# Kernel optimization log

Measured on AMD Instinct MI355X. Metric: run time of the kernel, lower is better.

The kernel has to match this reference:

```python
import jax, jax.numpy as jnp
import numpy as np

B, T, F, D, H, DFF, L = 8, 1024, 64, 512, 8, 2048, 3
DH = D // H
PERIODS = np.array([16, 256, 4096], np.int32)
CMS_LRS = np.array([0.01, 0.001, 0.0001], np.float32)
TITANS_LR = 0.01
TITANS_CLIP = 0.1


def layernorm(x, w, b):
    m = x.mean(-1, keepdims=True)
    v = x.var(-1, keepdims=True)
    return (x - m) * jax.lax.rsqrt(v + 1e-5) * w + b


def setup_inputs() -> dict:
    key = jax.random.key(0)
    ks = jax.random.split(key, 40)
    f32 = jnp.float32
    def rn(i, shape, s=0.02):
        return jax.random.normal(ks[i], shape, f32) * s
    inp = {
        'x': jax.random.normal(ks[0], (B, T, F), f32),
        'titans_W': jnp.zeros((D, D), f32),
        'cms_summary': jnp.zeros((L, D), f32),
        'cms_buf_sum': jnp.zeros((L, D), f32),
        'cms_count': jnp.zeros((L,), jnp.int32),
        'cms_step': jnp.zeros((L,), jnp.int32),
        'in_norm_w': jnp.ones((F,), f32), 'in_norm_b': jnp.zeros((F,), f32),
        'in_proj_W': rn(1, (D, F)), 'in_proj_b': jnp.zeros((D,), f32),
        'W_base': rn(2, (D, D), 0.01),
        'tit_out_W': rn(3, (D, D)), 'tit_out_b': jnp.zeros((D,), f32),
        'gate_W': rn(4, (L, D, D)), 'gate_b': jnp.zeros((L, D), f32),
        'comb_W': rn(5, (D, L * D)), 'comb_b': jnp.zeros((D,), f32),
        'n1_w': jnp.ones((D,), f32), 'n1_b': jnp.zeros((D,), f32),
        'qkv_W': rn(6, (3 * D, D)), 'qkv_b': jnp.zeros((3 * D,), f32),
        'ao_W': rn(7, (D, D)), 'ao_b': jnp.zeros((D,), f32),
        'n2_w': jnp.ones((D,), f32), 'n2_b': jnp.zeros((D,), f32),
        'f1_W': rn(8, (DFF, D)), 'f1_b': jnp.zeros((DFF,), f32),
        'f2_W': rn(9, (D, DFF)), 'f2_b': jnp.zeros((D,), f32),
        'fn_w': jnp.ones((D,), f32), 'fn_b': jnp.zeros((D,), f32),
        'head_W': rn(10, (1, D)), 'head_b': jnp.zeros((1,), f32),
    }
    return inp


def cms_tick_all(means, summary, buf_sum, count, step, gate_W, gate_b):
    """Sequential tick over T timesteps, vectorized over the L levels.
    means: [T, D] batch-mean of final hidden at each timestep."""
    periods = jnp.asarray(PERIODS)
    lrs = jnp.asarray(CMS_LRS)
    def step_fn(carry, m):
        summ, bs, cnt, stp = carry
        bs = bs + m[None, :]              # [L, D]
        cnt = cnt + 1
        stp = stp + 1
        fire = cnt >= periods              # [L]
        acc = bs / cnt.astype(bs.dtype)[:, None]
        g = jax.nn.sigmoid(jnp.einsum('lij,lj->li', gate_W, acc) + gate_b)
        new_summ = jnp.where(fire[:, None], (1.0 - lrs)[:, None] * summ + lrs[:, None] * g * acc, summ)
        bs = jnp.where(fire[:, None], jnp.zeros_like(bs), bs)
        cnt = jnp.where(fire, jnp.zeros_like(cnt), cnt)
        return (new_summ, bs, cnt, stp), None
    (summary, buf_sum, count, step), _ = jax.lax.scan(step_fn, (summary, buf_sum, count, step), means)
    return summary, buf_sum, count, step


def reference(x, titans_W, cms_summary, cms_buf_sum, cms_count, cms_step,
              in_norm_w, in_norm_b, in_proj_W, in_proj_b,
              W_base, tit_out_W, tit_out_b,
              gate_W, gate_b, comb_W, comb_b,
              n1_w, n1_b, qkv_W, qkv_b, ao_W, ao_b,
              n2_w, n2_b, f1_W, f1_b, f2_W, f2_b,
              fn_w, fn_b, head_W, head_b):
    # input norm + projection: [B,T,F] -> [B,T,D]
    h = layernorm(x, in_norm_w, in_norm_b) @ in_proj_W.T + in_proj_b
    # Titans fast-weight read
    W = W_base + titans_W
    tit = (h @ W.T) @ tit_out_W.T + tit_out_b
    # Titans fast-weight update (detached in the original)
    hs = jax.lax.stop_gradient(h)
    target = hs.mean(axis=1)               # [B, D]
    query = hs[:, -1, :]                   # [B, D]
    pred_m = query @ titans_W.T
    err = (target - pred_m).mean(axis=0)   # [D]
    grad = jnp.outer(err, query.mean(axis=0))
    gn = jnp.linalg.norm(grad)
    grad = jnp.where(gn > TITANS_CLIP, grad * (TITANS_CLIP / gn), grad)
    new_W = titans_W + TITANS_LR * grad
    h = h + tit
    # CMS residual from current summaries: concat [L*D] -> combine -> [D]
    cms_out = cms_summary.reshape(L * D) @ comb_W.T + comb_b
    h = h + cms_out                        # broadcast over [B,T,D]
    # transformer block (pre-norm, causal MHA)
    hn = layernorm(h, n1_w, n1_b)
    qkv = hn @ qkv_W.T + qkv_b
    q, k, v = jnp.split(qkv, 3, axis=-1)
    def to_heads(t):
        return t.reshape(B, T, H, DH).transpose(0, 2, 1, 3)
    q, k, v = to_heads(q), to_heads(k), to_heads(v)
    scores = jnp.einsum('bhqd,bhkd->bhqk', q, k) / np.sqrt(DH).astype(np.float32)
    causal = jnp.triu(jnp.ones((T, T), bool), 1)
    scores = jnp.where(causal, -jnp.inf, scores)
    attn = jax.nn.softmax(scores, axis=-1)
    ao = jnp.einsum('bhqk,bhkd->bhqd', attn, v).transpose(0, 2, 1, 3).reshape(B, T, D)
    h = h + ao @ ao_W.T + ao_b
    hn2 = layernorm(h, n2_w, n2_b)
    h = h + jax.nn.gelu(hn2 @ f1_W.T + f1_b, approximate=False) @ f2_W.T + f2_b
    h = layernorm(h, fn_w, fn_b)
    pred = (h @ head_W.T + head_b).squeeze(-1)   # [B, T]
    # CMS tick over all T steps (detached in the original)
    means = jax.lax.stop_gradient(h).mean(axis=0)  # [T, D]
    ns, nb, nc, nt = cms_tick_all(means, cms_summary, cms_buf_sum, cms_count, cms_step, gate_W, gate_b)
    return pred, new_W, ns, nb, nc, nt
```

## Files before the change

kernel.cpp:

```cpp
#include <hip/hip_runtime.h>
#include <hip/hip_bf16.h>
#include <math.h>

#define Bdim 8
#define Tdim 1024
#define Fdim 64
#define Ddim 512
#define Lcms 3

#define OFF_PRED 0
#define OFF_W    8192
#define OFF_NS   270336
#define OFF_NB   271872
#define OFF_NC   273408
#define OFF_NT   273411

typedef __hip_bfloat16 bf16;
typedef __attribute__((ext_vector_type(8))) short s8;
typedef __attribute__((ext_vector_type(4))) float f4;

__device__ __forceinline__ float b2f(bf16 v){ return __bfloat162float(v); }
__device__ __forceinline__ bf16  f2b(float v){ return __float2bfloat16(v); }
__device__ __forceinline__ short fb16(float v){ bf16 t = __float2bfloat16(v); return *reinterpret_cast<short*>(&t); }
__device__ __forceinline__ float toF(float v){ return v; }
__device__ __forceinline__ float toF(bf16 v){ return __bfloat162float(v); }
template<typename T> __device__ __forceinline__ T fromF(float v);
template<> __device__ __forceinline__ float fromF<float>(float v){ return v; }
template<> __device__ __forceinline__ bf16  fromF<bf16 >(float v){ return f2b(v); }

__device__ __forceinline__ f4 mfma16(s8 a, s8 b, f4 c){
  return __builtin_amdgcn_mfma_f32_16x16x32_bf16(a, b, c, 0, 0, 0);
}

__device__ __forceinline__ void gload16(const bf16* g, bf16* l){
  __builtin_amdgcn_global_load_lds(
      (const __attribute__((address_space(1))) unsigned*)g,
      (__attribute__((address_space(3))) unsigned*)l, 16, 0, 0);
}

__device__ __forceinline__ float gelu_fast(float x){
  float z2 = 1.5957691216f*(x + 0.044715f*x*x*x);
  z2 = fminf(fmaxf(z2, -18.f), 18.f);
  return x / (1.f + __expf(-z2));
}

__global__ __launch_bounds__(256) void k_conv_all(
    const void* s0, const void* s1, const void* s2, const void* s3,
    const void* s4, const void* s5, const void* s6, const void* s7,
    const void* s8v, const void* s9, const void* s10, const void* s11,
    const void* s12, const void* s13,
    bf16* __restrict__ dst, const unsigned* __restrict__ w1, int* __restrict__ flag,
    const int* __restrict__ cnt, int* __restrict__ params){
  bool isbf = (w1[0] == 0x3F803F80u);
  if (blockIdx.x==0 && threadIdx.x==0){
    flag[0] = isbf ? 1 : 0;
    const int P[3] = {16,256,4096};
    for (int l=0;l<3;l++){
      int c0 = cnt[l];
      int t1 = P[l] - c0 - 1; if (t1 < 0) t1 = 0;
      int K = (t1 >= Tdim) ? 0 : 1 + (Tdim-1-t1)/P[l];
      params[l*4+0]=t1; params[l*4+1]=K; params[l*4+2]=c0+t1+1; params[l*4+3]=c0;
    }
  }
  const void* srcs[14] = {s0,s1,s2,s3,s4,s5,s6,s7,s8v,s9,s10,s11,s12,s13};
  const int   ns[14]   = {262144,512,786432,1536,262144,512,1048576,2048,1048576,512,
                          32768,512,786432,1536};
  int gstride = gridDim.x*blockDim.x;
  int gid = blockIdx.x*blockDim.x + threadIdx.x;
  int base = 0;
  #pragma unroll
  for (int s=0;s<14;s++){
    int n = ns[s];
    if (isbf){
      const short* sp = (const short*)srcs[s]; short* dp = (short*)(dst+base);
      for (int i=gid;i<n;i+=gstride) dp[i] = sp[i];
    } else {
      const float* sp = (const float*)srcs[s];
      for (int i=gid;i<n;i+=gstride) dst[base+i] = f2b(sp[i]);
    }
    base += n;
  }
}

template<typename TW>
__device__ __forceinline__ void lnx_impl(const TW* x, const TW* nw, const TW* nb_, bf16* xn){
  int row = blockIdx.x*4 + (threadIdx.x>>6);
  int lane = threadIdx.x & 63;
  float v = toF(x[(size_t)row*Fdim + lane]);
  float s = v, s2 = v*v;
  #pragma unroll
  for (int off=32; off; off>>=1){ s += __shfl_down(s,off); s2 += __shfl_down(s2,off); }
  s = __shfl(s, 0); s2 = __shfl(s2, 0);
  float mu = s*(1.f/64.f);
  float var = s2*(1.f/64.f) - mu*mu;
  float rstd = rsqrtf(var + 1e-5f);
  xn[(size_t)row*Fdim + lane] = f2b((v-mu)*rstd*toF(nw[lane]) + toF(nb_[lane]));
}
__global__ __launch_bounds__(256) void k_lnx(const void* x, const void* nw, const void* nb_,
    bf16* xn, const int* flg){
  if (*flg) lnx_impl<bf16>((const bf16*)x,(const bf16*)nw,(const bf16*)nb_,xn);
  else      lnx_impl<float>((const float*)x,(const float*)nw,(const float*)nb_,xn);
}

__global__ __launch_bounds__(256) void k_reduce_tq1(const bf16* __restrict__ h,
    float* __restrict__ redtmp){
  int b = blockIdx.x>>5, chunk = blockIdx.x&31;
  int tid = threadIdx.x;
  #pragma unroll
  for (int o=0;o<2;o++){
    int d = tid + o*256;
    const bf16* p = h + ((size_t)b*Tdim + chunk*32)*Ddim + d;
    float s = 0.f;
    #pragma unroll
    for (int t=0;t<32;t++) s += b2f(p[(size_t)t*Ddim]);
    redtmp[((size_t)b*32 + chunk)*Ddim + d] = s;
  }
}

template<typename TW>
__device__ __forceinline__ void misc1_impl(const TW* Wbse, const TW* tW, bf16* Wout,
    const TW* summ, const TW* combW, const TW* combb, float* outv,
    const bf16* h, const float* redtmp, float* target, float* query){
  int blk = blockIdx.x, tid = threadIdx.x;
  if (blk < 1024){
    int i = blk*256 + tid;
    Wout[i] = f2b(toF(Wbse[i]) + toF(tW[i]));
  } else if (blk < 1152){
    __shared__ float s_s[Lcms*Ddim];
    for (int i=tid;i<Lcms*Ddim;i+=256) s_s[i] = toF(summ[i]);
    __syncthreads();
    int wave = tid>>6, lane = tid&63;
    int d = (blk-1024)*4 + wave;
    const TW* wr = combW + (size_t)d*(Lcms*Ddim);
    float a = 0.f;
    for (int j=lane;j<Lcms*Ddim;j+=64) a += s_s[j]*toF(wr[j]);
    #pragma unroll
    for (int off=32; off; off>>=1) a += __shfl_down(a,off);
    if (lane==0) outv[d] = a + toF(combb[d]);
  } else {
    int i = (blk-1152)*256 + tid;
    int b = i>>9, d = i&511;
    float s = 0.f;
    #pragma unroll
    for (int c=0;c<32;c++) s += redtmp[((size_t)b*32+c)*Ddim + d];
    target[i] = s*(1.f/(float)Tdim);
    query[i]  = b2f(h[((size_t)b*Tdim + (Tdim-1))*Ddim + d]);
  }
}
__global__ __launch_bounds__(256) void k_misc1(const void* Wbse, const void* tW, bf16* Wout,
    const void* summ, const void* combW, const void* combb, float* outv,
    const bf16* h, const float* redtmp, float* target, float* query, const int* flg){
  if (*flg) misc1_impl<bf16>((const bf16*)Wbse,(const bf16*)tW,Wout,(const bf16*)summ,
                             (const bf16*)combW,(const bf16*)combb,outv,h,redtmp,target,query);
  else      misc1_impl<float>((const float*)Wbse,(const float*)tW,Wout,(const float*)summ,
                             (const float*)combW,(const float*)combb,outv,h,redtmp,target,query);
}

template<typename TW>
__device__ __forceinline__ void titans_err_impl(const float* target, const float* query,
    const TW* tW, float* err, float* qmean){
  int wave = threadIdx.x>>6, lane = threadIdx.x&63;
  int d = blockIdx.x*4 + wave;
  const TW* wr = tW + (size_t)d*Ddim;
  float s = 0.f;
  #pragma unroll
  for (int b=0;b<Bdim;b++){
    const float* q = query + b*Ddim;
    float p = 0.f;
    for (int j=lane;j<Ddim;j+=64) p += q[j]*toF(wr[j]);
    s += p;
  }
  #pragma unroll
  for (int off=32; off; off>>=1) s += __shfl_down(s,off);
  if (lane==0){
    float e=0.f, qm=0.f;
    #pragma unroll
    for (int b=0;b<Bdim;b++){ e += target[b*Ddim+d]; qm += query[b*Ddim+d]; }
    err[d]   = (e - s)*(1.f/(float)Bdim);
    qmean[d] = qm*(1.f/(float)Bdim);
  }
}
__global__ __launch_bounds__(256) void k_titans_err(const float* target, const float* query,
    const void* tW, float* err, float* qmean, const int* flg){
  if (*flg) titans_err_impl<bf16>(target,query,(const bf16*)tW,err,qmean);
  else      titans_err_impl<float>(target,query,(const float*)tW,err,qmean);
}

template<typename TW>
__device__ __forceinline__ void new_W_impl(const TW* tW, const float* err, const float* qmean,
    TW* outW){
  int tid = threadIdx.x;
  float a = err[tid]*err[tid] + err[tid+256]*err[tid+256];
  float b = qmean[tid]*qmean[tid] + qmean[tid+256]*qmean[tid+256];
  #pragma unroll
  for (int off=32; off; off>>=1){ a += __shfl_down(a,off); b += __shfl_down(b,off); }
  __shared__ float sa[4], sb[4];
  int lane = tid & 63, wid = tid >> 6;
  if (lane==0){ sa[wid]=a; sb[wid]=b; }
  __syncthreads();
  float A = sa[0]+sa[1]+sa[2]+sa[3];
  float Bq= sb[0]+sb[1]+sb[2]+sb[3];
  float gn = sqrtf(A*Bq);
  float sf = 0.01f * (gn > 0.1f ? 0.1f/gn : 1.0f);
  int i = blockIdx.x*256 + tid;
  int r = i >> 9, c = i & 511;
  outW[i] = fromF<TW>(toF(tW[i]) + sf*err[r]*qmean[c]);
}
__global__ __launch_bounds__(256) void k_new_W(const void* tW, const float* err,
    const float* qmean, void* out, const int* flg){
  if (*flg) new_W_impl<bf16>((const bf16*)tW, err, qmean, ((bf16*)out)+OFF_W);
  else      new_W_impl<float>((const float*)tW, err, qmean, ((float*)out)+OFF_W);
}

template<int MODE, int DEPTH>
__global__ __launch_bounds__(512) void gemm_mfma(const bf16* __restrict__ A,
    const bf16* __restrict__ Bw, const bf16* __restrict__ bias,
    const float* __restrict__ colvec, bf16* __restrict__ Cout,
    const bf16* __restrict__ resid, int M, int N, int K){
  __shared__ __align__(16) bf16 As[DEPTH][128*32];
  __shared__ __align__(16) bf16 Bs[DEPTH][128*32];
  int tid = threadIdx.x, wave = tid>>6, lane = tid&63, quad = lane>>4, l16 = lane&15;
  int row0 = blockIdx.x*128, col0 = blockIdx.y*128;
  int wr = (wave>>2)*64, wc = (wave&3)*32;
  int srow = wave*16 + (lane>>2);
  int scol = (((lane&3) ^ ((lane>>3)&3)))*8;
  int rswz = (quad ^ ((l16>>1)&3))*8;
  f4 acc[8] = {};
  int niter = K >> 5;
  #define STAGE(bu, k0) { \
    gload16(A  + (size_t)(row0 + srow)*K + (k0) + scol, &As[bu][wave*512 + lane*8]); \
    gload16(Bw + (size_t)(col0 + srow)*K + (k0) + scol, &Bs[bu][wave*512 + lane*8]); \
  }
  STAGE(0, 0)
  if (DEPTH >= 3 && niter > 1) STAGE(1, 32)
  if (DEPTH >= 4 && niter > 2) STAGE(2, 64)
  for (int k=0; k<niter; k++){
    int bu = k & (DEPTH-1);
    if (DEPTH == 2){
      if (k+1 < niter){
        STAGE((k+1)&1, (k+1)<<5)
        asm volatile("s_waitcnt vmcnt(2)" ::: "memory");
      } else {
        asm volatile("s_waitcnt vmcnt(0)" ::: "memory");
      }
    } else {
      if (k+3 < niter){
        STAGE((k+3)&3, (k+3)<<5)
        asm volatile("s_waitcnt vmcnt(6)" ::: "memory");
      } else if (k+2 < niter){
        asm volatile("s_waitcnt vmcnt(4)" ::: "memory");
      } else if (k+1 < niter){
        asm volatile("s_waitcnt vmcnt(2)" ::: "memory");
      } else {
        asm volatile("s_waitcnt vmcnt(0)" ::: "memory");
      }
    }
    __builtin_amdgcn_s_barrier();
    s8 af[4], bfv[2];
    #pragma unroll
    for (int i=0;i<4;i++) af[i]  = *reinterpret_cast<const s8*>(&As[bu][(wr + i*16 + l16)*32 + rswz]);
    #pragma unroll
    for (int j=0;j<2;j++) bfv[j] = *reinterpret_cast<const s8*>(&Bs[bu][(wc + j*16 + l16)*32 + rswz]);
    #pragma unroll
    for (int i=0;i<4;i++)
      #pragma unroll
      for (int j=0;j<2;j++)
        acc[i*2+j] = mfma16(af[i], bfv[j], acc[i*2+j]);
    asm volatile("s_waitcnt lgkmcnt(0)" ::: "memory");
    __builtin_amdgcn_s_barrier();
  }
  #undef STAGE
  #pragma unroll
  for (int i=0;i<4;i++){
    #pragma unroll
    for (int j=0;j<2;j++){
      int n = col0 + wc + j*16 + l16;
      f4 a = acc[i*2+j];
      #pragma unroll
      for (int r=0;r<4;r++){
        int m = row0 + wr + i*16 + quad*4 + r;
        float v = a[r];
        if (MODE & 1) v += b2f(bias[n]);
        if (MODE & 8) v += colvec[n];
        if (MODE & 4) v = gelu_fast(v);
        if (MODE & 2) v += b2f(resid[(size_t)m*Ddim + n]);
        Cout[(size_t)m*N + n] = f2b(v);
      }
    }
  }
}

template<typename TW, int HEAD>
__device__ __forceinline__ void ln_impl(const bf16* in, const TW* w, const TW* b, bf16* outp,
    const TW* hw, const TW* hb, TW* pred){
  int row = blockIdx.x;
  const bf16* r = in + (size_t)row*Ddim;
  int tid = threadIdx.x;
  float v0 = b2f(r[tid]), v1 = b2f(r[tid + 256]);
  float s = v0+v1, s2 = v0*v0 + v1*v1;
  #pragma unroll
  for (int off=32; off; off>>=1){ s += __shfl_down(s,off); s2 += __shfl_down(s2,off); }
  __shared__ float sa[4], sb[4], sc[4];
  int lane = tid & 63, wid = tid >> 6;
  if (lane==0){ sa[wid]=s; sb[wid]=s2; }
  __syncthreads();
  float ts  = sa[0]+sa[1]+sa[2]+sa[3];
  float ts2 = sb[0]+sb[1]+sb[2]+sb[3];
  float mu = ts*(1.f/(float)Ddim);
  float var = ts2*(1.f/(float)Ddim) - mu*mu;
  float rstd = rsqrtf(var + 1e-5f);
  float o0 = (v0-mu)*rstd*toF(w[tid])     + toF(b[tid]);
  float o1 = (v1-mu)*rstd*toF(w[tid+256]) + toF(b[tid+256]);
  outp[(size_t)row*Ddim + tid]       = f2b(o0);
  outp[(size_t)row*Ddim + tid + 256] = f2b(o1);
  if (HEAD){
    float sp = o0*toF(hw[tid]) + o1*toF(hw[tid+256]);
    #pragma unroll
    for (int off=32; off; off>>=1) sp += __shfl_down(sp,off);
    if (lane==0) sc[wid] = sp;
    __syncthreads();
    if (tid==0) pred[row] = fromF<TW>(sc[0]+sc[1]+sc[2]+sc[3] + toF(hb[0]));
  }
}
template<int HEAD>
__global__ __launch_bounds__(256) void k_ln(const bf16* in, const void* w, const void* b,
    bf16* outp, const void* hw, const void* hb, void* out, const int* flg){
  if (*flg) ln_impl<bf16,HEAD>(in,(const bf16*)w,(const bf16*)b,outp,
                               (const bf16*)hw,(const bf16*)hb,((bf16*)out)+OFF_PRED);
  else      ln_impl<float,HEAD>(in,(const float*)w,(const float*)b,outp,
                               (const float*)hw,(const float*)hb,((float*)out)+OFF_PRED);
}

__global__ __launch_bounds__(256) void k_attn_mfma(const bf16* __restrict__ qkv,
                                                   bf16* __restrict__ ao){
  int blk = blockIdx.x;
  int bh = blk & 63;
  int qt = 15 - (blk >> 6);
  int head = bh & 7, b = bh >> 3;
  __shared__ __align__(16) bf16 Ks[64][72];
  __shared__ __align__(16) unsigned Vt4[64*36];
  __shared__ __align__(16) bf16 Ps[4][16][72];
  int tid = threadIdx.x, wave = tid>>6, lane = tid&63, quad = lane>>4, l16 = lane&15;
  int q0w = qt*64 + wave*16;
  const bf16* basep = qkv + (size_t)b*Tdim*1536 + head*64;
  s8 qf0 = *reinterpret_cast<const s8*>(basep + (size_t)(q0w+l16)*1536 + quad*8);
  s8 qf1 = *reinterpret_cast<const s8*>(basep + (size_t)(q0w+l16)*1536 + 32 + quad*8);
  f4 o[4] = {{0,0,0,0},{0,0,0,0},{0,0,0,0},{0,0,0,0}};
  float m_r[4] = {-3.0e38f,-3.0e38f,-3.0e38f,-3.0e38f};
  float l_r[4] = {0.f,0.f,0.f,0.f};
  int key_s = tid>>3, dgk = (tid&7)*8;
  int vp = tid>>3, dgv = (tid&7)*8;
  int vu4 = (((vp>>2) ^ (tid&7)) & 7)*4 + (vp&3);
  int nch = qt + 1;
  s8 kr0, kr1, vra, vrb;
  {
    const bf16* kp = basep + (size_t)key_s*1536 + 512 + dgk;
    kr0 = *reinterpret_cast<const s8*>(kp);
    kr1 = *reinterpret_cast<const s8*>(kp + (size_t)32*1536);
    const bf16* vpa = basep + (size_t)(2*vp)*1536 + 1024 + dgv;
    vra = *reinterpret_cast<const s8*>(vpa);
    vrb = *reinterpret_cast<const s8*>(vpa + 1536);
  }
  for (int ch=0; ch<nch; ch++){
    *reinterpret_cast<s8*>(&Ks[key_s][dgk])    = kr0;
    *reinterpret_cast<s8*>(&Ks[32+key_s][dgk]) = kr1;
    #pragma unroll
    for (int j=0;j<8;j++){
      unsigned w = (unsigned)(unsigned short)vra[j] | ((unsigned)(unsigned short)vrb[j] << 16);
      Vt4[(dgv+j)*36 + vu4] = w;
    }
    __syncthreads();
    if (ch+1 < nch){
      const bf16* kp = basep + (size_t)((ch+1)*64+key_s)*1536 + 512 + dgk;
      kr0 = *reinterpret_cast<const s8*>(kp);
      kr1 = *reinterpret_cast<const s8*>(kp + (size_t)32*1536);
      const bf16* vpa = basep + (size_t)((ch+1)*64 + 2*vp)*1536 + 1024 + dgv;
      vra = *reinterpret_cast<const s8*>(vpa);
      vrb = *reinterpret_cast<const s8*>(vpa + 1536);
    }
    f4 sc4[4] = {{0,0,0,0},{0,0,0,0},{0,0,0,0},{0,0,0,0}};
    #pragma unroll
    for (int t=0;t<4;t++){
      sc4[t] = mfma16(qf0, *reinterpret_cast<const s8*>(&Ks[t*16+l16][quad*8]),    sc4[t]);
      sc4[t] = mfma16(qf1, *reinterpret_cast<const s8*>(&Ks[t*16+l16][32+quad*8]), sc4[t]);
    }
    int key0 = ch*64 + l16;
    #pragma unroll
    for (int r=0;r<4;r++){
      int qrow = q0w + quad*4 + r;
      float a0 = (key0      <= qrow) ? sc4[0][r]*0.125f : -3.0e38f;
      float a1 = (key0 + 16 <= qrow) ? sc4[1][r]*0.125f : -3.0e38f;
      float a2 = (key0 + 32 <= qrow) ? sc4[2][r]*0.125f : -3.0e38f;
      float a3 = (key0 + 48 <= qrow) ? sc4[3][r]*0.125f : -3.0e38f;
      float mx = fmaxf(fmaxf(a0,a1), fmaxf(a2,a3));
      mx = fmaxf(mx, __shfl_xor(mx,1)); mx = fmaxf(mx, __shfl_xor(mx,2));
      mx = fmaxf(mx, __shfl_xor(mx,4)); mx = fmaxf(mx, __shfl_xor(mx,8));
      float mnew = fmaxf(m_r[r], mx);
      float al = __expf(m_r[r]-mnew); m_r[r] = mnew;
      float p0 = __expf(a0-mnew), p1 = __expf(a1-mnew);
      float p2 = __expf(a2-mnew), p3 = __expf(a3-mnew);
      float rs = (p0+p1)+(p2+p3);
      rs += __shfl_xor(rs,1); rs += __shfl_xor(rs,2);
      rs += __shfl_xor(rs,4); rs += __shfl_xor(rs,8);
      l_r[r] = l_r[r]*al + rs;
      o[0][r]*=al; o[1][r]*=al; o[2][r]*=al; o[3][r]*=al;
      int prow = quad*4+r;
      *reinterpret_cast<short*>(&Ps[wave][prow][l16])    = fb16(p0);
      *reinterpret_cast<short*>(&Ps[wave][prow][16+l16]) = fb16(p1);
      *reinterpret_cast<short*>(&Ps[wave][prow][32+l16]) = fb16(p2);
      *reinterpret_cast<short*>(&Ps[wave][prow][48+l16]) = fb16(p3);
    }
    asm volatile("s_waitcnt lgkmcnt(0)" ::: "memory");
    s8 pf0 = *reinterpret_cast<const s8*>(&Ps[wave][l16][quad*8]);
    s8 pf1 = *reinterpret_cast<const s8*>(&Ps[wave][l16][32+quad*8]);
    #pragma unroll
    for (int j=0;j<4;j++){
      int d = j*16 + l16;
      int swz = (d>>3) & 7;
      s8 b0 = *reinterpret_cast<const s8*>(&Vt4[d*36 + ((quad   ^ swz))*4]);
      s8 b1 = *reinterpret_cast<const s8*>(&Vt4[d*36 + (((4+quad)^ swz))*4]);
      o[j] = mfma16(pf0, b0, o[j]);
      o[j] = mfma16(pf1, b1, o[j]);
    }
    __syncthreads();
  }
  #pragma unroll
  for (int r=0;r<4;r++){
    float inv = 1.f/l_r[r];
    size_t rowb = (size_t)(b*Tdim + q0w + quad*4 + r)*Ddim + head*64;
    ao[rowb + l16]      = f2b(o[0][r]*inv);
    ao[rowb + 16 + l16] = f2b(o[1][r]*inv);
    ao[rowb + 32 + l16] = f2b(o[2][r]*inv);
    ao[rowb + 48 + l16] = f2b(o[3][r]*inv);
  }
}

__global__ void k_means(const bf16* __restrict__ h, float* __restrict__ means){
  int i = blockIdx.x*256 + threadIdx.x;
  float s = 0.f;
  #pragma unroll
  for (int b=0;b<Bdim;b++) s += b2f(h[(size_t)b*Tdim*Ddim + i]);
  means[i] = s*(1.f/(float)Bdim);
}

template<typename TW>
__device__ __forceinline__ void cms_acc_impl(const float* means, const TW* bs0,
    const int* params, float* acc, bf16* acch, float* tailtmp){
  int tid = threadIdx.x;
  if (blockIdx.x < 384){
    int l = blockIdx.x>>7, k = blockIdx.x&127;
    int K = params[l*4+1];
    if (k >= K){
      for (int d=tid; d<Ddim; d+=256) acch[((size_t)l*128+k)*Ddim + d] = f2b(0.f);
      return;
    }
    int t1 = params[l*4], cnt0 = params[l*4+2];
    const int P[3] = {16,256,4096};
    int lo = (k==0) ? 0 : t1 + (k-1)*P[l] + 1;
    int hi = t1 + k*P[l];
    float inv = 1.f/((k==0) ? (float)cnt0 : (float)P[l]);
    int lane = tid&63, strip = tid>>6;
    __shared__ float red[4][Ddim];
    float4 a0 = {0,0,0,0}, a1 = {0,0,0,0};
    for (int t=lo+strip; t<=hi; t+=4){
      const float4* row = (const float4*)(means + (size_t)t*Ddim);
      float4 v0 = row[lane], v1 = row[lane+64];
      a0.x+=v0.x; a0.y+=v0.y; a0.z+=v0.z; a0.w+=v0.w;
      a1.x+=v1.x; a1.y+=v1.y; a1.z+=v1.z; a1.w+=v1.w;
    }
    ((float4*)red[strip])[lane]    = a0;
    ((float4*)red[strip])[lane+64] = a1;
    __syncthreads();
    for (int d=tid; d<Ddim; d+=256){
      float s = red[0][d]+red[1][d]+red[2][d]+red[3][d];
      if (k==0) s += toF(bs0[l*Ddim+d]);
      float v = s*inv;
      acc[((size_t)l*65+k)*Ddim + d] = v;
      acch[((size_t)l*128+k)*Ddim + d] = f2b(v);
    }
  } else {
    int bb = blockIdx.x - 384;
    int l = bb>>5, chunk = bb&31;
    int t1 = params[l*4], K = params[l*4+1];
    const int P[3] = {16,256,4096};
    int lo = (K==0) ? 0 : t1 + (K-1)*P[l] + 1;
    int f = tid & 127, strip = tid >> 7;
    int tbeg = chunk*32, tend = tbeg + 32;
    if (tbeg < lo) tbeg = lo;
    float4 a = {0,0,0,0};
    for (int t=tbeg+strip; t<tend; t+=2){
      float4 v = ((const float4*)(means + (size_t)t*Ddim))[f];
      a.x+=v.x; a.y+=v.y; a.z+=v.z; a.w+=v.w;
    }
    __shared__ float4 redt[2][128];
    redt[strip][f] = a;
    __syncthreads();
    if (strip==0){
      float4 b = redt[1][f];
      a.x+=b.x; a.y+=b.y; a.z+=b.z; a.w+=b.w;
      ((float4*)(tailtmp + ((size_t)l*32 + chunk)*Ddim))[f] = a;
    }
  }
}
__global__ __launch_bounds__(256) void k_cms_acc(const float* means, const void* bs0,
    const int* params, float* acc, bf16* acch, float* tailtmp, const int* flg){
  if (*flg) cms_acc_impl<bf16>(means,(const bf16*)bs0,params,acc,acch,tailtmp);
  else      cms_acc_impl<float>(means,(const float*)bs0,params,acc,acch,tailtmp);
}

__global__ __launch_bounds__(256) void k_cms_gate_mfma(const bf16* __restrict__ accbh,
    const bf16* __restrict__ wg, const bf16* __restrict__ wgb, float* __restrict__ g){
  int l = blockIdx.y;
  const bf16* A  = accbh + (size_t)l*128*Ddim;
  const bf16* Bw = wg    + (size_t)l*Ddim*Ddim;
  __shared__ __align__(16) bf16 As[128*32];
  __shared__ __align__(16) bf16 Bs[128*32];
  int tid = threadIdx.x, wave = tid>>6, lane = tid&63, quad = lane>>4, l16 = lane&15;
  int col0 = blockIdx.x*128;
  int wr = (wave>>1)*64, wc = (wave&1)*64;
  int srow = lane>>2, scol = (lane&3)*8;
  f4 acc[16] = {};
  for (int k0=0; k0<Ddim; k0+=32){
    __syncthreads();
    #pragma unroll
    for (int it=0; it<2; it++){
      int c = wave*2 + it;
      gload16(A  + (size_t)(c*16 + srow)*Ddim + k0 + scol, &As[c*512 + lane*8]);
      gload16(Bw + (size_t)(col0 + c*16 + srow)*Ddim + k0 + scol, &Bs[c*512 + lane*8]);
    }
    __syncthreads();
    s8 af[4], bfv[4];
    #pragma unroll
    for (int i=0;i<4;i++) af[i]  = *reinterpret_cast<const s8*>(&As[(wr + i*16 + l16)*32 + quad*8]);
    #pragma unroll
    for (int j=0;j<4;j++) bfv[j] = *reinterpret_cast<const s8*>(&Bs[(wc + j*16 + l16)*32 + quad*8]);
    #pragma unroll
    for (int i=0;i<4;i++)
      #pragma unroll
      for (int j=0;j<4;j++)
        acc[i*4+j] = mfma16(af[i], bfv[j], acc[i*4+j]);
  }
  #pragma unroll
  for (int i=0;i<4;i++){
    #pragma unroll
    for (int j=0;j<4;j++){
      int n = col0 + wc + j*16 + l16;
      f4 a = acc[i*4+j];
      #pragma unroll
      for (int r=0;r<4;r++){
        int m = wr + i*16 + quad*4 + r;
        if (m < 65){
          float v = a[r] + b2f(wgb[l*Ddim + n]);
          g[((size_t)l*65 + m)*Ddim + n] = 1.f/(1.f + __expf(-v));
        }
      }
    }
  }
}

template<typename TW>
__device__ __forceinline__ void cms_final_impl(const float* acc, const float* g,
    const float* tailtmp, const TW* summ0, const TW* bs0, const int* params,
    const int* step0, TW* out){
  int l = blockIdx.x;
  int t1 = params[l*4], K = params[l*4+1], c0 = params[l*4+3];
  const int P[3] = {16,256,4096};
  const float LR[3] = {0.01f,0.001f,0.0001f};
  float lr = LR[l];
  for (int d=threadIdx.x; d<Ddim; d+=256){
    float s = toF(summ0[l*Ddim + d]);
    for (int k=0;k<K;k++)
      s = (1.f-lr)*s + lr*g[((size_t)l*65+k)*Ddim+d]*acc[((size_t)l*65+k)*Ddim+d];
    out[OFF_NS + l*Ddim + d] = fromF<TW>(s);
    float nbv = (K==0) ? toF(bs0[l*Ddim+d]) : 0.f;
    #pragma unroll
    for (int c=0;c<32;c++) nbv += tailtmp[((size_t)l*32+c)*Ddim + d];
    out[OFF_NB + l*Ddim + d] = fromF<TW>(nbv);
  }
  if (threadIdx.x==0){
    int nc = (K==0) ? c0 + Tdim : (Tdim-1 - (t1 + (K-1)*P[l]));
    out[OFF_NC + l] = fromF<TW>((float)nc);
    out[OFF_NT + l] = fromF<TW>((float)(step0[l] + Tdim));
  }
}
__global__ __launch_bounds__(256) void k_cms_final(const float* acc, const float* g,
    const float* tailtmp, const void* summ0, const void* bs0, const int* params,
    const int* step0, void* out, const int* flg){
  if (*flg) cms_final_impl<bf16>(acc,g,tailtmp,(const bf16*)summ0,(const bf16*)bs0,params,step0,(bf16*)out);
  else      cms_final_impl<float>(acc,g,tailtmp,(const float*)summ0,(const float*)bs0,params,step0,(float*)out);
}

extern "C" void kernel_launch(void* const* d_in, const int* in_sizes, int n_in,
                              void* d_out, int out_size, void* d_ws, size_t ws_size,
                              hipStream_t stream) {
  (void)in_sizes; (void)n_in; (void)out_size; (void)ws_size;
  const void* x           = d_in[0];
  const void* titansW     = d_in[1];
  const void* cms_summary = d_in[2];
  const void* cms_bufsum  = d_in[3];
  const int*  cms_count   = (const int*)d_in[4];
  const int*  cms_step    = (const int*)d_in[5];
  const void* in_norm_w   = d_in[6];
  const void* in_norm_b   = d_in[7];
  const void* in_proj_W   = d_in[8];
  const void* in_proj_b   = d_in[9];
  const void* W_base      = d_in[10];
  const void* tit_out_W   = d_in[11];
  const void* tit_out_b   = d_in[12];
  const void* gate_W      = d_in[13];
  const void* gate_b      = d_in[14];
  const void* comb_W      = d_in[15];
  const void* comb_b      = d_in[16];
  const void* n1_w        = d_in[17];
  const void* n1_b        = d_in[18];
  const void* qkv_W       = d_in[19];
  const void* qkv_b       = d_in[20];
  const void* ao_W        = d_in[21];
  const void* ao_b        = d_in[22];
  const void* n2_w        = d_in[23];
  const void* n2_b        = d_in[24];
  const void* f1_W        = d_in[25];
  const void* f1_b        = d_in[26];
  const void* f2_W        = d_in[27];
  const void* f2_b        = d_in[28];
  const void* fn_w        = d_in[29];
  const void* fn_b        = d_in[30];
  const void* head_W      = d_in[31];
  const void* head_b      = d_in[32];

  char* u8 = (char*)d_ws;
  bf16*  h     = (bf16*)(u8 + 0);
  bf16*  hnA   = (bf16*)(u8 + 8388608);
  bf16*  big   = (bf16*)(u8 + 16777216);
  bf16*  xn    = big;
  bf16*  tmid  = big + (size_t)8192*1536;
  float* means = (float*)(u8 + 50331648);
  bf16*  Wb    = (bf16*)(u8 + 52428800);
  bf16*  wall  = (bf16*)(u8 + 52953088);
  bf16*  wtit  = wall;
  bf16*  wtitb = wall + 262144;
  bf16*  wqkv  = wall + 262656;
  bf16*  wqkvb = wall + 1049088;
  bf16*  wao   = wall + 1050624;
  bf16*  waob  = wall + 1312768;
  bf16*  wf1   = wall + 1313280;
  bf16*  wf1b  = wall + 2361856;
  bf16*  wf2   = wall + 2363904;
  bf16*  wf2b  = wall + 3412480;
  bf16*  wproj = wall + 3412992;
  bf16*  wprojb= wall + 3445760;
  bf16*  wgate = wall + 3446272;
  bf16*  wgateb= wall + 4232704;
  float* target= (float*)(u8 + 61421568);
  float* query = (float*)(u8 + 61437952);
  float* errv  = (float*)(u8 + 61454336);
  float* qmean = (float*)(u8 + 61456384);
  float* cmsout= (float*)(u8 + 61458944);
  float* accb  = (float*)(u8 + 61460992);
  float* gbuf  = (float*)(u8 + 61860352);
  bf16*  accbh = (bf16*) (u8 + 62259712);
  int*   params= (int*)  (u8 + 62652928);
  int*   dflag = (int*)  (u8 + 62652992);
  float* redtmp= (float*)(u8 + 62659584);
  float* tailtmp=(float*)(u8 + 63183872);

  k_conv_all<<<1024, 256, 0, stream>>>(tit_out_W, tit_out_b, qkv_W, qkv_b, ao_W, ao_b,
                                       f1_W, f1_b, f2_W, f2_b, in_proj_W, in_proj_b,
                                       gate_W, gate_b, wall, (const unsigned*)in_norm_w,
                                       dflag, cms_count, params);
  k_lnx<<<2048, 256, 0, stream>>>(x, in_norm_w, in_norm_b, xn, dflag);
  gemm_mfma<1,2><<<dim3(64,4), 512, 0, stream>>>(xn, wproj, wprojb, nullptr, h, nullptr, 8192, 512, 64);
  k_reduce_tq1<<<256, 256, 0, stream>>>(h, redtmp);
  k_misc1<<<1168, 256, 0, stream>>>(W_base, titansW, Wb, cms_summary, comb_W, comb_b,
                                    cmsout, h, redtmp, target, query, dflag);
  k_titans_err<<<128, 256, 0, stream>>>(target, query, titansW, errv, qmean, dflag);
  k_new_W<<<1024, 256, 0, stream>>>(titansW, errv, qmean, d_out, dflag);
  gemm_mfma<0,4><<<dim3(64,4), 512, 0, stream>>>(h, Wb, nullptr, nullptr, tmid, nullptr, 8192, 512, 512);
  gemm_mfma<11,4><<<dim3(64,4), 512, 0, stream>>>(tmid, wtit, wtitb, cmsout, h, h, 8192, 512, 512);
  k_ln<0><<<8192, 256, 0, stream>>>(h, n1_w, n1_b, hnA, nullptr, nullptr, nullptr, dflag);
  gemm_mfma<1,2><<<dim3(64,12), 512, 0, stream>>>(hnA, wqkv, wqkvb, nullptr, big, nullptr, 8192, 1536, 512);
  k_attn_mfma<<<1024, 256, 0, stream>>>(big, tmid);
  gemm_mfma<3,4><<<dim3(64,4), 512, 0, stream>>>(tmid, wao, waob, nullptr, h, h, 8192, 512, 512);
  k_ln<0><<<8192, 256, 0, stream>>>(h, n2_w, n2_b, hnA, nullptr, nullptr, nullptr, dflag);
  gemm_mfma<5,2><<<dim3(64,16), 512, 0, stream>>>(hnA, wf1, wf1b, nullptr, big, nullptr, 8192, 2048, 512);
  gemm_mfma<3,4><<<dim3(64,4), 512, 0, stream>>>(big, wf2, wf2b, nullptr, h, h, 8192, 512, 2048);
  k_ln<1><<<8192, 256, 0, stream>>>(h, fn_w, fn_b, hnA, head_W, head_b, d_out, dflag);
  k_means<<<2048, 256, 0, stream>>>(hnA, means);
  k_cms_acc<<<480, 256, 0, stream>>>(means, cms_bufsum, params, accb, accbh, tailtmp, dflag);
  k_cms_gate_mfma<<<dim3(4,3), 256, 0, stream>>>(accbh, wgate, wgateb, gbuf);
  k_cms_final<<<Lcms, 256, 0, stream>>>(accb, gbuf, tailtmp, cms_summary, cms_bufsum, params, cms_step, d_out, dflag);
}
```

Before: 450.8 us.

## Process two K/V chunks per barrier in attention kernel with double LDS buffers

Restructures the flash-attention loop so two 64-key chunks are staged into LDS together and computed between a single pair of barriers, with register prefetch of the next two chunks. This halves the number of __syncthreads per key range and gives more global-load latency hiding. In exchange it doubles the K/V LDS footprint and the prefetch registers, which may reduce occupancy.

```diff
diff --git a/kernel.cpp b/kernel.cpp
--- a/kernel.cpp
+++ b/kernel.cpp
@@ -337,8 +337,8 @@
   int bh = blk & 63;
   int qt = 15 - (blk >> 6);
   int head = bh & 7, b = bh >> 3;
-  __shared__ __align__(16) bf16 Ks[64][72];
-  __shared__ __align__(16) unsigned Vt4[64*36];
+  __shared__ __align__(16) bf16 Ks[2][64][72];
+  __shared__ __align__(16) unsigned Vt4[2][64*36];
   __shared__ __align__(16) bf16 Ps[4][16][72];
   int tid = threadIdx.x, wave = tid>>6, lane = tid&63, quad = lane>>4, l16 = lane&15;
   int q0w = qt*64 + wave*16;
@@ -352,37 +352,29 @@
   int vp = tid>>3, dgv = (tid&7)*8;
   int vu4 = (((vp>>2) ^ (tid&7)) & 7)*4 + (vp&3);
   int nch = qt + 1;
-  s8 kr0, kr1, vra, vrb;
+  s8 kr0[2], kr1[2], vra[2], vrb[2];
   {
     const bf16* kp = basep + (size_t)key_s*1536 + 512 + dgk;
-    kr0 = *reinterpret_cast<const s8*>(kp);
-    kr1 = *reinterpret_cast<const s8*>(kp + (size_t)32*1536);
+    kr0[0] = *reinterpret_cast<const s8*>(kp);
+    kr1[0] = *reinterpret_cast<const s8*>(kp + (size_t)32*1536);
     const bf16* vpa = basep + (size_t)(2*vp)*1536 + 1024 + dgv;
-    vra = *reinterpret_cast<const s8*>(vpa);
-    vrb = *reinterpret_cast<const s8*>(vpa + 1536);
-  }
-  for (int ch=0; ch<nch; ch++){
-    *reinterpret_cast<s8*>(&Ks[key_s][dgk])    = kr0;
-    *reinterpret_cast<s8*>(&Ks[32+key_s][dgk]) = kr1;
-    #pragma unroll
-    for (int j=0;j<8;j++){
-      unsigned w = (unsigned)(unsigned short)vra[j] | ((unsigned)(unsigned short)vrb[j] << 16);
-      Vt4[(dgv+j)*36 + vu4] = w;
-    }
-    __syncthreads();
-    if (ch+1 < nch){
-      const bf16* kp = basep + (size_t)((ch+1)*64+key_s)*1536 + 512 + dgk;
-      kr0 = *reinterpret_cast<const s8*>(kp);
-      kr1 = *reinterpret_cast<const s8*>(kp + (size_t)32*1536);
-      const bf16* vpa = basep + (size_t)((ch+1)*64 + 2*vp)*1536 + 1024 + dgv;
-      vra = *reinterpret_cast<const s8*>(vpa);
-      vrb = *reinterpret_cast<const s8*>(vpa + 1536);
-    }
+    vra[0] = *reinterpret_cast<const s8*>(vpa);
+    vrb[0] = *reinterpret_cast<const s8*>(vpa + 1536);
+    if (1 < nch){
+      const bf16* kp1 = basep + (size_t)(64+key_s)*1536 + 512 + dgk;
+      kr0[1] = *reinterpret_cast<const s8*>(kp1);
+      kr1[1] = *reinterpret_cast<const s8*>(kp1 + (size_t)32*1536);
+      const bf16* vpa1 = basep + (size_t)(64 + 2*vp)*1536 + 1024 + dgv;
+      vra[1] = *reinterpret_cast<const s8*>(vpa1);
+      vrb[1] = *reinterpret_cast<const s8*>(vpa1 + 1536);
+    }
+  }
+  auto do_chunk = [&](int ch, int bu){
     f4 sc4[4] = {{0,0,0,0},{0,0,0,0},{0,0,0,0},{0,0,0,0}};
     #pragma unroll
     for (int t=0;t<4;t++){
-      sc4[t] = mfma16(qf0, *reinterpret_cast<const s8*>(&Ks[t*16+l16][quad*8]),    sc4[t]);
-      sc4[t] = mfma16(qf1, *reinterpret_cast<const s8*>(&Ks[t*16+l16][32+quad*8]), sc4[t]);
+      sc4[t] = mfma16(qf0, *reinterpret_cast<const s8*>(&Ks[bu][t*16+l16][quad*8]),    sc4[t]);
+      sc4[t] = mfma16(qf1, *reinterpret_cast<const s8*>(&Ks[bu][t*16+l16][32+quad*8]), sc4[t]);
     }
     int key0 = ch*64 + l16;
     #pragma unroll
@@ -417,12 +409,41 @@
     for (int j=0;j<4;j++){
       int d = j*16 + l16;
       int swz = (d>>3) & 7;
-      s8 b0 = *reinterpret_cast<const s8*>(&Vt4[d*36 + ((quad   ^ swz))*4]);
-      s8 b1 = *reinterpret_cast<const s8*>(&Vt4[d*36 + (((4+quad)^ swz))*4]);
+      s8 b0 = *reinterpret_cast<const s8*>(&Vt4[bu][d*36 + ((quad   ^ swz))*4]);
+      s8 b1 = *reinterpret_cast<const s8*>(&Vt4[bu][d*36 + (((4+quad)^ swz))*4]);
       o[j] = mfma16(pf0, b0, o[j]);
       o[j] = mfma16(pf1, b1, o[j]);
     }
+  };
+  for (int ch0=0; ch0<nch; ch0+=2){
+    #pragma unroll
+    for (int s=0;s<2;s++){
+      if (ch0+s < nch){
+        *reinterpret_cast<s8*>(&Ks[s][key_s][dgk])    = kr0[s];
+        *reinterpret_cast<s8*>(&Ks[s][32+key_s][dgk]) = kr1[s];
+        #pragma unroll
+        for (int j=0;j<8;j++){
+          unsigned w = (unsigned)(unsigned short)vra[s][j] | ((unsigned)(unsigned short)vrb[s][j] << 16);
+          Vt4[s][(dgv+j)*36 + vu4] = w;
+        }
+      }
+    }
     __syncthreads();
+    #pragma unroll
+    for (int s=0;s<2;s++){
+      int chn = ch0 + 2 + s;
+      if (chn < nch){
+        const bf16* kp = basep + (size_t)(chn*64+key_s)*1536 + 512 + dgk;
+        kr0[s] = *reinterpret_cast<const s8*>(kp);
+        kr1[s] = *reinterpret_cast<const s8*>(kp + (size_t)32*1536);
+        const bf16* vpa = basep + (size_t)(chn*64 + 2*vp)*1536 + 1024 + dgv;
+        vra[s] = *reinterpret_cast<const s8*>(vpa);
+        vrb[s] = *reinterpret_cast<const s8*>(vpa + 1536);
+      }
+    }
+    do_chunk(ch0, 0);
+    if (ch0+1 < nch) do_chunk(ch0+1, 1);
+    if (ch0+2 < nch) __syncthreads();
   }
   #pragma unroll
   for (int r=0;r<4;r++){
```

Measured after the change: 442.8 us. Within noise of the previous version (-1.8%).
